# Kernel optimization log

Hardware: AMD Instinct MI355X
Metric: run time of the kernel (lower is better)

The kernel has to match this reference:

```python
import jax, jax.numpy as jnp
import numpy as np

B, S, D = 16, 2048, 512
E, TOP_K = 8, 2
H = 4 * D  # expert hidden dim


def setup_inputs() -> dict:
    key = jax.random.key(0)
    ks = jax.random.split(key, 8)
    x = jax.random.normal(ks[0], (B, S, D), dtype=jnp.float32)
    gate_w = jax.random.normal(ks[1], (D, E), dtype=jnp.float32) * 0.02
    gate_b = jnp.zeros((E,), dtype=jnp.float32)
    w1 = jax.random.normal(ks[2], (E, D, H), dtype=jnp.float32) * 0.02
    b1 = jnp.zeros((E, H), dtype=jnp.float32)
    w2 = jax.random.normal(ks[3], (E, H, D), dtype=jnp.float32) * 0.02
    b2 = jnp.zeros((E, D), dtype=jnp.float32)
    return {"x": x, "gate_w": gate_w, "gate_b": gate_b,
            "w1": w1, "b1": b1, "w2": w2, "b2": b2}


def reference(x, gate_w, gate_b, w1, b1, w2, b2):
    # Sample-level top-k routing (mean pooling over sequence).
    b, s, d = x.shape
    e = gate_b.shape[0]
    pooled = x.mean(axis=1)                       # [B, D]
    logits = pooled @ gate_w + gate_b             # [B, E]
    top_v, top_i = jax.lax.top_k(logits, TOP_K)   # [B, K]
    weights = jax.nn.softmax(top_v, axis=-1)      # [B, K]
    # Dense per-sample-per-expert combine weight; zero for unselected experts,
    # which makes the dense expert evaluation below mathematically identical
    # to the masked gather/scatter in the torch module.
    w_full = jnp.zeros((b, e), dtype=x.dtype).at[jnp.arange(b)[:, None], top_i].add(weights)
    out = jnp.zeros_like(x)
    for ex in range(e):  # small fixed expert loop
        h = jax.nn.gelu(x @ w1[ex] + b1[ex], approximate=False)  # torch GELU default = exact erf
        y = h @ w2[ex] + b2[ex]  # Dropout(0.1) is identity in eval mode
        out = out + y * w_full[:, ex][:, None, None]
    return out
```

## Files before the change

kernel.cpp:

```cpp
#include <hip/hip_runtime.h>
#include <hip/hip_bf16.h>
#include <math.h>

#define B_ 16
#define S_ 2048
#define D_ 512
#define E_ 8
#define H_ 2048

typedef __bf16 bf16_t;
typedef __bf16 bf16x8 __attribute__((ext_vector_type(8)));
typedef __bf16 bf16x4v __attribute__((ext_vector_type(4)));
typedef float f32x4 __attribute__((ext_vector_type(4)));

__device__ __forceinline__ void gload_lds16(const void* g, void* l) {
  __builtin_amdgcn_global_load_lds((const __attribute__((address_space(1))) void*)g,
                                   (__attribute__((address_space(3))) void*)l,
                                   16, 0, 0);
}

#define BAR() __builtin_amdgcn_s_barrier()
#define LGKM0() do { asm volatile("s_waitcnt lgkmcnt(0)" ::: "memory"); \
                     __builtin_amdgcn_sched_barrier(0); } while (0)
#define LGKMW() asm volatile("s_waitcnt lgkmcnt(0)" ::: "memory")
#define VM4() asm volatile("s_waitcnt vmcnt(4)" ::: "memory")
#define VM0() asm volatile("s_waitcnt vmcnt(0)" ::: "memory")
#define PRIO1() __builtin_amdgcn_s_setprio(1)
#define PRIO0() __builtin_amdgcn_s_setprio(0)

__device__ __forceinline__ float fast_gelu(float v) {
  const float t = 1.5957691216f * v * (1.0f + 0.044715f * v * v);
  return v * __builtin_amdgcn_rcpf(1.0f + __expf(-t));
}

__global__ void prep_kernel(const float* __restrict__ x, bf16_t* __restrict__ xbf,
                            float* __restrict__ pool,
                            const float* __restrict__ w1, bf16_t* __restrict__ w1t,
                            const float* __restrict__ w2, bf16_t* __restrict__ w2t) {
  const int id = blockIdx.x;
  const int tid = threadIdx.x;
  if (id < 256) {
    const int ch = id & 15, b = id >> 4;
    const int cg = tid & 127;
    const int rg = tid >> 7;
    const size_t base = ((size_t)b * S_ + (size_t)ch * 128 + rg * 32) * D_ + cg * 4;
    const float* xp = x + base;
    bf16_t* op = xbf + base;
    float s0 = 0.f, s1 = 0.f, s2 = 0.f, s3 = 0.f;
#pragma unroll 4
    for (int r = 0; r < 32; ++r) {
      float4 v = *reinterpret_cast<const float4*>(xp + (size_t)r * D_);
      s0 += v.x; s1 += v.y; s2 += v.z; s3 += v.w;
      bf16x4v o;
      o[0] = (bf16_t)v.x; o[1] = (bf16_t)v.y; o[2] = (bf16_t)v.z; o[3] = (bf16_t)v.w;
      *reinterpret_cast<bf16x4v*>(op + (size_t)r * D_) = o;
    }
    float* pp = pool + ((size_t)b * 64 + ch * 4 + rg) * D_ + cg * 4;
    pp[0] = s0; pp[1] = s1; pp[2] = s2; pp[3] = s3;
    return;
  }
  __shared__ bf16_t tile[128][72];
  int t = id - 256;
  const float* in; bf16_t* outp; int R, C, r0, c0;
  if (t < 1024) {
    const int e = t >> 7, u = t & 127;
    R = D_; C = H_;
    r0 = (u >> 4) * 64; c0 = (u & 15) * 128;
    in = w1 + (size_t)e * R * C; outp = w1t + (size_t)e * R * C;
  } else {
    t -= 1024;
    const int e = t >> 7, u = t & 127;
    R = H_; C = D_;
    r0 = (u >> 2) * 64; c0 = (u & 3) * 128;
    in = w2 + (size_t)e * R * C; outp = w2t + (size_t)e * R * C;
  }
  const int tx = tid & 15, ty = (tid >> 4) & 15, hf = tid >> 8;
#pragma unroll
  for (int i = 0; i < 4; ++i) {
    const int r = r0 + ty + i * 16;
    float4 v = *reinterpret_cast<const float4*>(&in[(size_t)r * C + c0 + hf * 64 + tx * 4]);
    tile[hf * 64 + tx * 4 + 0][ty + i * 16] = (bf16_t)v.x;
    tile[hf * 64 + tx * 4 + 1][ty + i * 16] = (bf16_t)v.y;
    tile[hf * 64 + tx * 4 + 2][ty + i * 16] = (bf16_t)v.z;
    tile[hf * 64 + tx * 4 + 3][ty + i * 16] = (bf16_t)v.w;
  }
  __syncthreads();
#pragma unroll
  for (int i = 0; i < 4; ++i) {
    const int c = c0 + hf * 64 + ty + i * 16;
    bf16x4v o;
    o[0] = tile[hf * 64 + ty + i * 16][tx * 4 + 0];
    o[1] = tile[hf * 64 + ty + i * 16][tx * 4 + 1];
    o[2] = tile[hf * 64 + ty + i * 16][tx * 4 + 2];
    o[3] = tile[hf * 64 + ty + i * 16][tx * 4 + 3];
    *reinterpret_cast<bf16x4v*>(&outp[(size_t)c * R + r0 + tx * 4]) = o;
  }
}

__global__ void gate_kernel(const float* __restrict__ pool, const float* __restrict__ gw,
                            const float* __restrict__ gb, int* __restrict__ route_e,
                            float* __restrict__ route_w) {
  const int b = blockIdx.x;
  const int d = threadIdx.x;
  float p = 0.f;
#pragma unroll
  for (int c = 0; c < 64; ++c) p += pool[((size_t)b * 64 + c) * D_ + d];
  p *= (1.0f / (float)S_);

  __shared__ float red[512];
  __shared__ float logits[E_];
  for (int e = 0; e < E_; ++e) {
    red[d] = p * gw[d * E_ + e];
    __syncthreads();
    for (int off = 256; off > 0; off >>= 1) {
      if (d < off) red[d] += red[d + off];
      __syncthreads();
    }
    if (d == 0) logits[e] = red[0] + gb[e];
    __syncthreads();
  }
  if (d == 0) {
    int i0 = 0; float v0 = logits[0];
    for (int e = 1; e < E_; ++e) if (logits[e] > v0) { v0 = logits[e]; i0 = e; }
    int i1 = -1; float v1 = -3.0e38f;
    for (int e = 0; e < E_; ++e) if (e != i0 && logits[e] > v1) { v1 = logits[e]; i1 = e; }
    const float z = expf(v1 - v0);
    const float inv = 1.0f / (1.0f + z);
    route_e[2 * b] = i0; route_e[2 * b + 1] = i1;
    route_w[2 * b] = inv; route_w[2 * b + 1] = z * inv;
  }
}

#define GEMM_THREAD_CONSTS() \
  const int tid = threadIdx.x; \
  const int lane = tid & 63; \
  const int wave = tid >> 6; \
  const int wr = wave >> 2; \
  const int wc = wave & 3; \
  const int fl = lane & 15; \
  const int hi = (lane >> 4) & 3; \
  const int flb = fl * 128; \
  const int xorv = (fl & 7) << 4; \
  const int koff0 = (hi * 16) ^ xorv; \
  const int koff1 = (64 + hi * 16) ^ xorv; \
  const int r0s = tid >> 3; \
  const int g0s = ((tid & 7) ^ (r0s & 7)) << 3; \
  const int r1s = 64 + (tid >> 3); \
  const int g1s = ((tid & 7) ^ (r1s & 7)) << 3;

#define STAGE_HALF(g, ld, row0, col0, lo) do { \
  gload_lds16((g) + (size_t)((row0) + r0s) * (ld) + (col0) + g0s, smem + (lo) + tid * 16); \
  gload_lds16((g) + (size_t)((row0) + r1s) * (ld) + (col0) + g1s, smem + (lo) + 8192 + tid * 16); \
} while (0)

#define RD_A(mh) do { \
  const char* _pA = smem + ((((t) & 1) * 2 + wr) << 14); \
  _Pragma("unroll") for (int mq = 0; mq < 4; ++mq) { \
    a[mq][0] = *reinterpret_cast<const bf16x8*>(_pA + (mh) * 8192 + mq * 2048 + flb + koff0); \
    a[mq][1] = *reinterpret_cast<const bf16x8*>(_pA + (mh) * 8192 + mq * 2048 + flb + koff1); \
  } } while (0)

#define RD_B(nh) do { \
  const char* _pB = smem + 65536 + ((((t) & 1) * 2 + (wc >> 1)) << 14) + ((wc & 1) << 13); \
  _Pragma("unroll") for (int nq = 0; nq < 2; ++nq) { \
    bb[nh][nq][0] = *reinterpret_cast<const bf16x8*>(_pB + (nh) * 4096 + nq * 2048 + flb + koff0); \
    bb[nh][nq][1] = *reinterpret_cast<const bf16x8*>(_pB + (nh) * 4096 + nq * 2048 + flb + koff1); \
  } } while (0)

#define MFMA_Q(mh, nh) do { \
  _Pragma("unroll") for (int mq = 0; mq < 4; ++mq) \
  _Pragma("unroll") for (int nq = 0; nq < 2; ++nq) { \
    acc[(mh)*4+mq][(nh)*2+nq] = __builtin_amdgcn_mfma_f32_16x16x32_bf16( \
        a[mq][0], bb[nh][nq][0], acc[(mh)*4+mq][(nh)*2+nq], 0, 0, 0); \
    acc[(mh)*4+mq][(nh)*2+nq] = __builtin_amdgcn_mfma_f32_16x16x32_bf16( \
        a[mq][1], bb[nh][nq][1], acc[(mh)*4+mq][(nh)*2+nq], 0, 0, 0); \
  } } while (0)

__global__ __launch_bounds__(512, 2) void gemm1_kernel(
    const bf16_t* __restrict__ xbf, const bf16_t* __restrict__ w1t,
    const float* __restrict__ b1, const int* __restrict__ route_e,
    bf16_t* __restrict__ h_ws, int g0) {
  __shared__ alignas(16) char smem[131072];
  const int nwg = gridDim.x;
  const int id = blockIdx.x;
  const int swz = (id & 7) * (nwg >> 3) + (id >> 3);
  const int lg = swz >> 6;
  const int tile = swz & 63;
  const int m0 = (tile >> 3) * 256;
  const int n0 = (tile & 7) * 256;
  const int g = g0 + lg;
  const int b = g >> 1;
  const int e = route_e[g];
  const bf16_t* Ax = xbf + (size_t)b * S_ * D_;
  const bf16_t* Bw = w1t + (size_t)e * H_ * D_;
  bf16_t* C = h_ws + (size_t)lg * S_ * H_;

  GEMM_THREAD_CONSTS();

  f32x4 acc[8][4];
#pragma unroll
  for (int i = 0; i < 8; ++i)
#pragma unroll
    for (int j = 0; j < 4; ++j) acc[i][j] = f32x4{0.f, 0.f, 0.f, 0.f};
  bf16x8 a[4][2], bb[2][2][2];

#define ST_A1(tt, hh) STAGE_HALF(Ax, D_, m0 + (hh) * 128, (tt) * 64, ((((tt) & 1) * 2 + (hh)) << 14))
#define ST_B1(tt, hh) STAGE_HALF(Bw, D_, n0 + (hh) * 128, (tt) * 64, 65536 + ((((tt) & 1) * 2 + (hh)) << 14))

  const int NT = D_ / 64;
  ST_A1(0, 0); ST_A1(0, 1); ST_B1(0, 0); ST_B1(0, 1);
  ST_B1(1, 0); ST_B1(1, 1);
  VM4(); BAR();

  for (int t = 0; t < NT; ++t) {
    RD_A(0); RD_B(0);
    if (t + 1 < NT) ST_A1(t + 1, 0);
    BAR(); LGKM0(); PRIO1(); MFMA_Q(0, 0); PRIO0(); BAR();
    RD_B(1);
    if (t + 1 < NT) ST_A1(t + 1, 1);
    BAR(); LGKM0(); PRIO1(); MFMA_Q(0, 1); PRIO0(); BAR();
    RD_A(1);
    if (t + 2 < NT) ST_B1(t + 2, 0);
    BAR(); LGKM0(); PRIO1(); MFMA_Q(1, 0); PRIO0(); BAR();
    if (t + 2 < NT) ST_B1(t + 2, 1);
    if (t < NT - 2) { VM4(); } else if (t == NT - 2) { VM0(); }
    BAR(); PRIO1(); MFMA_Q(1, 1); PRIO0(); BAR();
  }
#undef ST_A1
#undef ST_B1

  const int rb2 = hi * 4;
#pragma unroll
  for (int ni = 0; ni < 4; ++ni) {
    const int col = wc * 64 + ni * 16 + fl;
    const float bias = b1[e * H_ + n0 + col];
    const int cb = col * 2;
#pragma unroll
    for (int mi = 0; mi < 8; ++mi) {
#pragma unroll
      for (int j = 0; j < 4; ++j) {
        const int row = wr * 128 + mi * 16 + rb2 + j;
        const float v = acc[mi][ni][j] + bias;
        const int ad = (row << 9) + (cb ^ (((row >> 2) & 3) << 5));
        *reinterpret_cast<bf16_t*>(smem + ad) = (bf16_t)fast_gelu(v);
      }
    }
  }
  LGKMW(); BAR();
#pragma unroll
  for (int i = 0; i < 16; ++i) {
    const int byte = i * 8192 + tid * 16;
    const int row = byte >> 9;
    const int colb = byte & 511;
    const int ad = (row << 9) + (colb ^ (((row >> 2) & 3) << 5));
    const bf16x8 vv = *reinterpret_cast<const bf16x8*>(smem + ad);
    *reinterpret_cast<bf16x8*>((char*)C + ((size_t)(m0 + row) * H_ + n0) * 2 + colb) = vv;
  }
}

__global__ __launch_bounds__(512, 2) void gemm2_kernel(
    const bf16_t* __restrict__ h_ws, const bf16_t* __restrict__ w2t,
    const float* __restrict__ b2, const int* __restrict__ route_e,
    const float* __restrict__ route_w, float* __restrict__ out, int b0) {
  __shared__ alignas(16) char smem[131072];
  const int nwg = gridDim.x;
  const int id = blockIdx.x;
  const int swz = (id & 7) * (nwg >> 3) + (id >> 3);
  const int lb = swz >> 4;
  const int tile = swz & 15;
  const int m0 = (tile >> 1) * 256;
  const int n0 = (tile & 1) * 256;
  const int smp = b0 + lb;
  const int e0 = route_e[2 * smp], e1 = route_e[2 * smp + 1];
  const float wg0 = route_w[2 * smp], wg1 = route_w[2 * smp + 1];
  const float ratio = wg1 / wg0;
  const bf16_t* Ae1 = h_ws + (size_t)(lb * 2 + 1) * S_ * H_;
  const bf16_t* Ae0 = h_ws + (size_t)(lb * 2 + 0) * S_ * H_;
  const bf16_t* Be1 = w2t + (size_t)e1 * D_ * H_;
  const bf16_t* Be0 = w2t + (size_t)e0 * D_ * H_;

  GEMM_THREAD_CONSTS();

  f32x4 acc[8][4];
#pragma unroll
  for (int i = 0; i < 8; ++i)
#pragma unroll
    for (int j = 0; j < 4; ++j) acc[i][j] = f32x4{0.f, 0.f, 0.f, 0.f};
  bf16x8 a[4][2], bb[2][2][2];

#define ST_A2(tt, hh) do { const bf16_t* _ab = ((tt) < 32) ? Ae1 : Ae0; \
  STAGE_HALF(_ab, H_, m0 + (hh) * 128, ((tt) & 31) * 64, ((((tt) & 1) * 2 + (hh)) << 14)); } while (0)
#define ST_B2(tt, hh) do { const bf16_t* _bbp = ((tt) < 32) ? Be1 : Be0; \
  STAGE_HALF(_bbp, H_, n0 + (hh) * 128, ((tt) & 31) * 64, 65536 + ((((tt) & 1) * 2 + (hh)) << 14)); } while (0)

  const int NT = 64;
  ST_A2(0, 0); ST_A2(0, 1); ST_B2(0, 0); ST_B2(0, 1);
  ST_B2(1, 0); ST_B2(1, 1);
  VM4(); BAR();

  for (int t = 0; t < NT; ++t) {
    RD_A(0); RD_B(0);
    if (t + 1 < NT) ST_A2(t + 1, 0);
    BAR(); LGKM0(); PRIO1(); MFMA_Q(0, 0); PRIO0(); BAR();
    RD_B(1);
    if (t + 1 < NT) ST_A2(t + 1, 1);
    BAR(); LGKM0(); PRIO1(); MFMA_Q(0, 1); PRIO0(); BAR();
    RD_A(1);
    if (t + 2 < NT) ST_B2(t + 2, 0);
    BAR(); LGKM0(); PRIO1(); MFMA_Q(1, 0); PRIO0(); BAR();
    if (t + 2 < NT) ST_B2(t + 2, 1);
    if (t < NT - 2) { VM4(); } else if (t == NT - 2) { VM0(); }
    BAR(); PRIO1(); MFMA_Q(1, 1); PRIO0();
    if (t == 31) {
#pragma unroll
      for (int i = 0; i < 8; ++i)
#pragma unroll
        for (int j = 0; j < 4; ++j) acc[i][j] = acc[i][j] * ratio;
    }
    BAR();
  }
#undef ST_A2
#undef ST_B2

  const int rb2 = hi * 4;
  float* Co = out + (size_t)smp * S_ * D_;
#pragma unroll
  for (int p = 0; p < 2; ++p) {
#pragma unroll
    for (int ni = 0; ni < 4; ++ni) {
      const int col = wc * 64 + ni * 16 + fl;
      const float wb = wg0 * b2[e0 * D_ + n0 + col] + wg1 * b2[e1 * D_ + n0 + col];
      const int cb = col * 4;
#pragma unroll
      for (int mq = 0; mq < 4; ++mq) {
        const int mi = 4 * p + mq;
#pragma unroll
        for (int j = 0; j < 4; ++j) {
          const int row = wr * 128 + mi * 16 + rb2 + j;
          const int lrow = (row & 63) + ((row >> 7) << 6);
          const int ad = (lrow << 10) + (cb ^ (((row >> 2) & 1) << 6));
          *reinterpret_cast<float*>(smem + ad) = wg0 * acc[mi][ni][j] + wb;
        }
      }
    }
    LGKMW(); BAR();
#pragma unroll
    for (int i = 0; i < 16; ++i) {
      const int byte = i * 8192 + tid * 16;
      const int lrow = byte >> 10;
      const int colb = byte & 1023;
      const int row = (lrow & 63) + ((lrow >> 6) << 7) + p * 64;
      const int ad = (lrow << 10) + (colb ^ (((row >> 2) & 1) << 6));
      const f32x4 vv = *reinterpret_cast<const f32x4*>(smem + ad);
      *reinterpret_cast<f32x4*>((char*)Co + ((size_t)(m0 + row) * D_ + n0) * 4 + colb) = vv;
    }
    LGKMW(); BAR();
  }
}

extern "C" void kernel_launch(void* const* d_in, const int* in_sizes, int n_in,
                              void* d_out, int out_size, void* d_ws, size_t ws_size,
                              hipStream_t stream) {
  const float* x      = (const float*)d_in[0];
  const float* gate_w = (const float*)d_in[1];
  const float* gate_b = (const float*)d_in[2];
  const float* w1     = (const float*)d_in[3];
  const float* b1     = (const float*)d_in[4];
  const float* w2     = (const float*)d_in[5];
  const float* b2     = (const float*)d_in[6];
  float* out = (float*)d_out;
  char* ws = (char*)d_ws;

  bf16_t* xbf    = (bf16_t*)(ws);
  bf16_t* w1t    = (bf16_t*)(ws + 33554432);
  bf16_t* w2t    = (bf16_t*)(ws + 50331648);
  float*  pool   = (float*)(ws + 67108864);
  int*    route_e = (int*)(ws + 69206016);
  float*  route_w = (float*)(ws + 69206144);
  const size_t h_off = 69206272;
  bf16_t* h_ws   = (bf16_t*)(ws + h_off);

  const size_t per_b = (size_t)2 * S_ * H_ * sizeof(bf16_t);
  size_t avail = (ws_size > h_off) ? (ws_size - h_off) : 0;
  int nb = (int)(avail / per_b);
  if (nb < 1) nb = 1;
  if (nb > B_) nb = B_;

  prep_kernel<<<2304, 512, 0, stream>>>(x, xbf, pool, w1, w1t, w2, w2t);
  gate_kernel<<<B_, 512, 0, stream>>>(pool, gate_w, gate_b, route_e, route_w);

  for (int b0 = 0; b0 < B_; b0 += nb) {
    const int cb = (B_ - b0 < nb) ? (B_ - b0) : nb;
    gemm1_kernel<<<64 * cb * 2, 512, 0, stream>>>(xbf, w1t, b1, route_e, h_ws, b0 * 2);
    gemm2_kernel<<<16 * cb, 512, 0, stream>>>(h_ws, w2t, b2, route_e, route_w, out, b0);
  }
}
```

Measured before the change: 469.3 us.

## Use wave-shuffle gate reduction, add early LDS wait, store GEMM2 output directly

The gate kernel's tree reduction, which needed many barriers, becomes a per-wave shuffle reduction followed by a small cross-wave sum. The GEMM2 main loop gets an extra partial lgkmcnt wait before the first barrier. The epilogue no longer stages results through LDS for coalesced float4 stores and writes each accumulator element straight to global memory. That removes LDS round trips and barriers, but the stores become scattered 4-byte writes that coalesce less well.

New measurement: 464.7 us. No clear change (-1.0%).

```diff
diff --git a/kernel.cpp b/kernel.cpp
--- a/kernel.cpp
+++ b/kernel.cpp
@@ -23,6 +23,7 @@
 #define LGKM0() do { asm volatile("s_waitcnt lgkmcnt(0)" ::: "memory"); \
                      __builtin_amdgcn_sched_barrier(0); } while (0)
 #define LGKMW() asm volatile("s_waitcnt lgkmcnt(0)" ::: "memory")
+#define LGKM8() asm volatile("s_waitcnt lgkmcnt(8)" ::: "memory")
 #define VM4() asm volatile("s_waitcnt vmcnt(4)" ::: "memory")
 #define VM0() asm volatile("s_waitcnt vmcnt(0)" ::: "memory")
 #define PRIO1() __builtin_amdgcn_s_setprio(1)
@@ -102,23 +103,29 @@
                             float* __restrict__ route_w) {
   const int b = blockIdx.x;
   const int d = threadIdx.x;
+  const int lane = d & 63, wave = d >> 6;
   float p = 0.f;
 #pragma unroll
   for (int c = 0; c < 64; ++c) p += pool[((size_t)b * 64 + c) * D_ + d];
   p *= (1.0f / (float)S_);
 
-  __shared__ float red[512];
+  __shared__ float wsum[8][8];
   __shared__ float logits[E_];
+#pragma unroll
   for (int e = 0; e < E_; ++e) {
-    red[d] = p * gw[d * E_ + e];
-    __syncthreads();
-    for (int off = 256; off > 0; off >>= 1) {
-      if (d < off) red[d] += red[d + off];
-      __syncthreads();
-    }
-    if (d == 0) logits[e] = red[0] + gb[e];
-    __syncthreads();
-  }
+    float v = p * gw[d * E_ + e];
+#pragma unroll
+    for (int off = 32; off >= 1; off >>= 1) v += __shfl_xor(v, off);
+    if (lane == 0) wsum[wave][e] = v;
+  }
+  __syncthreads();
+  if (d < E_) {
+    float l = gb[d];
+#pragma unroll
+    for (int w = 0; w < 8; ++w) l += wsum[w][d];
+    logits[d] = l;
+  }
+  __syncthreads();
   if (d == 0) {
     int i0 = 0; float v0 = logits[0];
     for (int e = 1; e < E_; ++e) if (logits[e] > v0) { v0 = logits[e]; i0 = e; }
@@ -301,7 +308,7 @@
   for (int t = 0; t < NT; ++t) {
     RD_A(0); RD_B(0);
     if (t + 1 < NT) ST_A2(t + 1, 0);
-    BAR(); LGKM0(); PRIO1(); MFMA_Q(0, 0); PRIO0(); BAR();
+    LGKM8(); BAR(); LGKM0(); PRIO1(); MFMA_Q(0, 0); PRIO0(); BAR();
     RD_B(1);
     if (t + 1 < NT) ST_A2(t + 1, 1);
     BAR(); LGKM0(); PRIO1(); MFMA_Q(0, 1); PRIO0(); BAR();
@@ -325,36 +332,17 @@
   const int rb2 = hi * 4;
   float* Co = out + (size_t)smp * S_ * D_;
 #pragma unroll
-  for (int p = 0; p < 2; ++p) {
-#pragma unroll
-    for (int ni = 0; ni < 4; ++ni) {
-      const int col = wc * 64 + ni * 16 + fl;
-      const float wb = wg0 * b2[e0 * D_ + n0 + col] + wg1 * b2[e1 * D_ + n0 + col];
-      const int cb = col * 4;
-#pragma unroll
-      for (int mq = 0; mq < 4; ++mq) {
-        const int mi = 4 * p + mq;
-#pragma unroll
-        for (int j = 0; j < 4; ++j) {
-          const int row = wr * 128 + mi * 16 + rb2 + j;
-          const int lrow = (row & 63) + ((row >> 7) << 6);
-          const int ad = (lrow << 10) + (cb ^ (((row >> 2) & 1) << 6));
-          *reinterpret_cast<float*>(smem + ad) = wg0 * acc[mi][ni][j] + wb;
-        }
+  for (int ni = 0; ni < 4; ++ni) {
+    const int gc = n0 + wc * 64 + ni * 16 + fl;
+    const float wb = wg0 * b2[e0 * D_ + gc] + wg1 * b2[e1 * D_ + gc];
+#pragma unroll
+    for (int mi = 0; mi < 8; ++mi) {
+#pragma unroll
+      for (int j = 0; j < 4; ++j) {
+        const int gr = m0 + wr * 128 + mi * 16 + rb2 + j;
+        Co[(size_t)gr * D_ + gc] = wg0 * acc[mi][ni][j] + wb;
       }
     }
-    LGKMW(); BAR();
-#pragma unroll
-    for (int i = 0; i < 16; ++i) {
-      const int byte = i * 8192 + tid * 16;
-      const int lrow = byte >> 10;
-      const int colb = byte & 1023;
-      const int row = (lrow & 63) + ((lrow >> 6) << 7) + p * 64;
-      const int ad = (lrow << 10) + (colb ^ (((row >> 2) & 1) << 6));
-      const f32x4 vv = *reinterpret_cast<const f32x4*>(smem + ad);
-      *reinterpret_cast<f32x4*>((char*)Co + ((size_t)(m0 + row) * D_ + n0) * 4 + colb) = vv;
-    }
-    LGKMW(); BAR();
   }
 }
 
```
